# Optimization experiments

Measured on AMD Instinct MI355X. Metric: run time of the kernel, lower is better.

The kernel has to match this reference:

```python
import jax, jax.numpy as jnp
import numpy as np

B, T, C, H = 2, 2048, 1024, 16
D = C // H  # head dim = 64

def setup_inputs() -> dict:
    key = jax.random.key(0)
    ks = jax.random.split(key, 5)
    s = 0.02
    return {
        "x": jax.random.normal(ks[0], (B, T, C), dtype=jnp.float32),
        "Wqkv": jax.random.normal(ks[1], (C, 3 * C), dtype=jnp.float32) * s,
        "bqkv": jnp.zeros((3 * C,), dtype=jnp.float32),
        "Wproj": jax.random.normal(ks[2], (C, C), dtype=jnp.float32) * s,
        "bproj": jnp.zeros((C,), dtype=jnp.float32),
    }

def reference(x, Wqkv, bqkv, Wproj, bproj):
    b, t, c = x.shape
    qkv = x @ Wqkv + bqkv                       # [B,T,3C]
    q, k, v = jnp.split(qkv, 3, axis=-1)
    # [B,T,C] -> [B,H,T,D]
    q = q.reshape(b, t, H, D).transpose(0, 2, 1, 3)
    k = k.reshape(b, t, H, D).transpose(0, 2, 1, 3)
    v = v.reshape(b, t, H, D).transpose(0, 2, 1, 3)
    scale = 1.0 / np.sqrt(D).astype(np.float32)
    attn = jnp.einsum('bhqd,bhkd->bhqk', q, k) * scale  # [B,H,T,T]
    causal = jnp.tril(jnp.ones((t, t), dtype=bool))
    attn = jnp.where(causal, attn, jnp.float32(-jnp.inf))
    attn = jax.nn.softmax(attn, axis=-1)
    y = jnp.einsum('bhqk,bhkd->bhqd', attn, v)          # [B,H,T,D]
    y = y.transpose(0, 2, 1, 3).reshape(b, t, c)        # [B,T,C]
    return y @ Wproj + bproj
```

## Files before the change

### kernel.cpp

```cpp
#include <hip/hip_runtime.h>
#include <stdint.h>

#define B_ 2
#define T_ 2048
#define C_ 1024
#define H_ 16
#define D_ 64
#define M_ (B_*T_)
#define BHTD_ (B_*H_*T_*D_)

typedef __bf16 bf16x8 __attribute__((ext_vector_type(8)));
typedef __bf16 bf16x4 __attribute__((ext_vector_type(4)));
typedef __bf16 bf16x2 __attribute__((ext_vector_type(2)));
typedef float f32x4 __attribute__((ext_vector_type(4)));
typedef float f32x16 __attribute__((ext_vector_type(16)));

static __device__ __forceinline__ unsigned short f32_bf16(float f) {
    unsigned int u = __float_as_uint(f);
    u += 0x7FFFu + ((u >> 16) & 1u);
    return (unsigned short)(u >> 16);
}

static __device__ __forceinline__ int pack_bf16_2(float a, float b) {
    bf16x2 v = {(__bf16)a, (__bf16)b};
    return __builtin_bit_cast(int, v);
}

__global__ void cast_kernel(const float* __restrict__ in, unsigned short* __restrict__ out, int n) {
    int i = (blockIdx.x * 256 + threadIdx.x) * 4;
    if (i >= n) return;
    float4 f = *(const float4*)(in + i);
    ushort4 o;
    o.x = f32_bf16(f.x); o.y = f32_bf16(f.y); o.z = f32_bf16(f.z); o.w = f32_bf16(f.w);
    *(ushort4*)(out + i) = o;
}

__global__ void transpose_cast_kernel(const float* __restrict__ W, unsigned short* __restrict__ Wt,
                                      int K, int N) {
    __shared__ float tile[32][33];
    int n0 = blockIdx.x * 32, k0 = blockIdx.y * 32;
    int tx = threadIdx.x, ty = threadIdx.y;
    #pragma unroll
    for (int j = 0; j < 32; j += 8)
        tile[ty + j][tx] = W[(size_t)(k0 + ty + j) * N + n0 + tx];
    __syncthreads();
    #pragma unroll
    for (int j = 0; j < 32; j += 8)
        Wt[(size_t)(n0 + ty + j) * K + k0 + tx] = f32_bf16(tile[tx][ty + j]);
}

template<int EPI>
__global__ __launch_bounds__(256) void gemm_bt(
    const unsigned short* __restrict__ A,
    const unsigned short* __restrict__ Bt,
    const float* __restrict__ bias,
    unsigned short* __restrict__ out_bf16,
    float* __restrict__ out_f32,
    int M, int N, int K)
{
    __shared__ unsigned short As[2][128 * 32];
    __shared__ unsigned short Bs[2][128 * 32];
    int tid = threadIdx.x;
    int lane = tid & 63, wid = tid >> 6;
    int fr = lane & 15, fg = lane >> 4;
    int row0 = blockIdx.x * 128, col0 = blockIdx.y * 128;
    int wm = (wid >> 1) * 64, wn = (wid & 1) * 64;

    f32x4 acc[4][4];
    #pragma unroll
    for (int i = 0; i < 4; ++i)
        #pragma unroll
        for (int j = 0; j < 4; ++j)
            acc[i][j] = (f32x4){0.f, 0.f, 0.f, 0.f};

    const int srw = lane >> 2;
    const int scl = (lane & 3) * 8;
    const int c0 = wid * 2, c1 = wid * 2 + 1;

    auto stage = [&](int buf, int k0) {
        __builtin_amdgcn_global_load_lds(
            (const __attribute__((address_space(1))) void*)(A + (size_t)(row0 + c0 * 16 + srw) * K + k0 + scl),
            (__attribute__((address_space(3))) void*)(As[buf] + c0 * 512), 16, 0, 0);
        __builtin_amdgcn_global_load_lds(
            (const __attribute__((address_space(1))) void*)(A + (size_t)(row0 + c1 * 16 + srw) * K + k0 + scl),
            (__attribute__((address_space(3))) void*)(As[buf] + c1 * 512), 16, 0, 0);
        __builtin_amdgcn_global_load_lds(
            (const __attribute__((address_space(1))) void*)(Bt + (size_t)(col0 + c0 * 16 + srw) * K + k0 + scl),
            (__attribute__((address_space(3))) void*)(Bs[buf] + c0 * 512), 16, 0, 0);
        __builtin_amdgcn_global_load_lds(
            (const __attribute__((address_space(1))) void*)(Bt + (size_t)(col0 + c1 * 16 + srw) * K + k0 + scl),
            (__attribute__((address_space(3))) void*)(Bs[buf] + c1 * 512), 16, 0, 0);
    };

    stage(0, 0);
    __syncthreads();

    int cur = 0;
    for (int k0 = 0; k0 < K; k0 += 32) {
        if (k0 + 32 < K) stage(cur ^ 1, k0 + 32);

        bf16x8 af[4], bfr[4];
        #pragma unroll
        for (int i = 0; i < 4; ++i) {
            af[i]  = *(const bf16x8*)(As[cur] + (wm + i * 16 + fr) * 32 + fg * 8);
            bfr[i] = *(const bf16x8*)(Bs[cur] + (wn + i * 16 + fr) * 32 + fg * 8);
        }
        #pragma unroll
        for (int mi = 0; mi < 4; ++mi)
            #pragma unroll
            for (int ni = 0; ni < 4; ++ni)
                acc[mi][ni] = __builtin_amdgcn_mfma_f32_16x16x32_bf16(af[mi], bfr[ni], acc[mi][ni], 0, 0, 0);

        __syncthreads();
        cur ^= 1;
    }

    #pragma unroll
    for (int mi = 0; mi < 4; ++mi) {
        int rowb = row0 + wm + mi * 16 + fg * 4;
        #pragma unroll
        for (int ni = 0; ni < 4; ++ni) {
            int col = col0 + wn + ni * 16 + fr;
            float bv = bias[col];
            #pragma unroll
            for (int r = 0; r < 4; ++r) {
                float v = acc[mi][ni][r] + bv;
                int rr = rowb + r;
                if (EPI == 0) {
                    int part = col >> 10, c = col & 1023;
                    int h = c >> 6, d = c & 63;
                    int b = rr >> 11, t = rr & 2047;
                    if (part == 0) v *= 0.18033688011112042f;
                    size_t idx;
                    if (part == 2)
                        idx = (size_t)2 * BHTD_ + ((size_t)(b * H_ + h) * D_ + d) * T_ + t;
                    else
                        idx = (size_t)part * BHTD_ + ((size_t)(b * H_ + h) * T_ + t) * D_ + d;
                    out_bf16[idx] = f32_bf16(v);
                } else {
                    out_f32[(size_t)rr * N + col] = v;
                }
            }
        }
    }
}

__global__ __launch_bounds__(128) void attn_kernel(
    const unsigned short* __restrict__ qg,
    const unsigned short* __restrict__ kg,
    const unsigned short* __restrict__ vtg,
    unsigned short* __restrict__ y)
{
    const int id = blockIdx.x;
    const int xcd = id & 7, j = id >> 3;
    const int c = j & 31, g = j >> 5;
    int chunk;
    if      (g == 0) chunk = 31 - c;
    else if (g == 1) chunk = c;
    else if (g == 2) chunk = (15 - c) & 31;
    else             chunk = (c + 16) & 31;
    const int bh = xcd * 4 + (c >> 3);
    const int b = bh >> 4, h = bh & 15;
    const int tid = threadIdx.x, wid = tid >> 6, lane = tid & 63;
    const int lq = lane & 31, hi = lane >> 5;

    const unsigned short* qp = qg + (size_t)bh * (T_ * D_);
    const char* kpB = (const char*)(kg + (size_t)bh * (T_ * D_));
    const char* vpB = (const char*)(vtg + (size_t)bh * (D_ * T_));

    __shared__ __align__(16) char Ks[2][8192];
    __shared__ __align__(16) char Vs[2][8192];

    const int r0 = chunk * 64 + wid * 32;
    const int ntk = chunk + 1;

    bf16x8 qf[4];
    #pragma unroll
    for (int ds = 0; ds < 4; ++ds)
        qf[ds] = *(const bf16x8*)(qp + (size_t)(r0 + lq) * D_ + ds * 16 + hi * 8);

    f32x16 oT0, oT1;
    #pragma unroll
    for (int e = 0; e < 16; ++e) { oT0[e] = 0.f; oT1[e] = 0.f; }
    float lrun = 0.f;

    const int srow8 = lane >> 3;
    const int scol  = (lane & 7) * 16;
    const int ssw   = srow8 << 4;

    auto stage = [&](int buf, int kv0) {
        #pragma unroll
        for (int blk = 0; blk < 4; ++blk) {
            const int rbase = wid * 32 + blk * 8;
            __builtin_amdgcn_global_load_lds(
                (const __attribute__((address_space(1))) void*)
                    (kpB + (size_t)(kv0 + rbase + srow8) * 128 + (scol ^ ssw)),
                (__attribute__((address_space(3))) void*)(Ks[buf] + rbase * 128), 16, 0, 0);
            __builtin_amdgcn_global_load_lds(
                (const __attribute__((address_space(1))) void*)
                    (vpB + (size_t)(rbase + srow8) * 4096 + kv0 * 2 + (scol ^ ssw)),
                (__attribute__((address_space(3))) void*)(Vs[buf] + rbase * 128), 16, 0, 0);
        }
    };

    auto make_pb = [&](const f32x16& p, int g4a) -> bf16x8 {
        int A0 = pack_bf16_2(p[g4a * 4 + 0], p[g4a * 4 + 1]);
        int A1 = pack_bf16_2(p[g4a * 4 + 2], p[g4a * 4 + 3]);
        int B0 = pack_bf16_2(p[g4a * 4 + 4], p[g4a * 4 + 5]);
        int B1 = pack_bf16_2(p[g4a * 4 + 6], p[g4a * 4 + 7]);
        auto ra = __builtin_amdgcn_permlane32_swap(A0, B0, false, false);
        auto rb = __builtin_amdgcn_permlane32_swap(A1, B1, false, false);
        int4 w;
        w.x = ra[0]; w.y = rb[0]; w.z = ra[1]; w.w = rb[1];
        return __builtin_bit_cast(bf16x8, w);
    };

    stage(0, 0);
    __syncthreads();

    const int lsw = (lq & 7) << 4;
    int cur = 0;
    for (int t = 0; t < ntk; ++t) {
        const int kv0 = t * 64;
        if (t + 1 < ntk) stage(cur ^ 1, kv0 + 64);

        const char* Kb = Ks[cur];
        const char* Vb = Vs[cur];
        const bool diag = (t == chunk);
        const bool do_n1 = !(diag && wid == 0);

        f32x16 s0, s1;
        #pragma unroll
        for (int e = 0; e < 16; ++e) { s0[e] = 0.f; s1[e] = 0.f; }
        #pragma unroll
        for (int ds = 0; ds < 4; ++ds) {
            bf16x8 kf = *(const bf16x8*)(Kb + lq * 128 + ((ds * 32 + hi * 16) ^ lsw));
            s0 = __builtin_amdgcn_mfma_f32_32x32x16_bf16(kf, qf[ds], s0, 0, 0, 0);
        }
        if (do_n1) {
            #pragma unroll
            for (int ds = 0; ds < 4; ++ds) {
                bf16x8 kf = *(const bf16x8*)(Kb + (32 + lq) * 128 + ((ds * 32 + hi * 16) ^ lsw));
                s1 = __builtin_amdgcn_mfma_f32_32x32x16_bf16(kf, qf[ds], s1, 0, 0, 0);
            }
        }

        bf16x8 vf[2][4];
        #pragma unroll
        for (int dd = 0; dd < 2; ++dd)
            #pragma unroll
            for (int st = 0; st < 2; ++st)
                vf[dd][st] = *(const bf16x8*)(Vb + (dd * 32 + lq) * 128 +
                                              ((st * 32 + hi * 16) ^ lsw));
        if (do_n1) {
            #pragma unroll
            for (int dd = 0; dd < 2; ++dd)
                #pragma unroll
                for (int st = 2; st < 4; ++st)
                    vf[dd][st] = *(const bf16x8*)(Vb + (dd * 32 + lq) * 128 +
                                                  ((st * 32 + hi * 16) ^ lsw));
        }

        const int qrow = r0 + lq;
        if (diag && wid == 0) {
            #pragma unroll
            for (int e = 0; e < 16; ++e) {
                const int kvl = (e & 3) + ((e >> 2) << 3) + hi * 4;
                s0[e] = exp2f((kv0 + kvl <= qrow) ? s0[e] : -1e30f);
            }
        } else {
            #pragma unroll
            for (int e = 0; e < 16; ++e) s0[e] = exp2f(s0[e]);
        }
        {
            float a0 = (s0[0] + s0[1]) + (s0[2] + s0[3]);
            float a1 = (s0[4] + s0[5]) + (s0[6] + s0[7]);
            float a2 = (s0[8] + s0[9]) + (s0[10] + s0[11]);
            float a3 = (s0[12] + s0[13]) + (s0[14] + s0[15]);
            lrun += (a0 + a1) + (a2 + a3);
        }
        if (do_n1) {
            if (diag) {
                #pragma unroll
                for (int e = 0; e < 16; ++e) {
                    const int kvl = 32 + (e & 3) + ((e >> 2) << 3) + hi * 4;
                    s1[e] = exp2f((kv0 + kvl <= qrow) ? s1[e] : -1e30f);
                }
            } else {
                #pragma unroll
                for (int e = 0; e < 16; ++e) s1[e] = exp2f(s1[e]);
            }
            float a0 = (s1[0] + s1[1]) + (s1[2] + s1[3]);
            float a1 = (s1[4] + s1[5]) + (s1[6] + s1[7]);
            float a2 = (s1[8] + s1[9]) + (s1[10] + s1[11]);
            float a3 = (s1[12] + s1[13]) + (s1[14] + s1[15]);
            lrun += (a0 + a1) + (a2 + a3);
        }

        {
            bf16x8 pb = make_pb(s0, 0);
            oT0 = __builtin_amdgcn_mfma_f32_32x32x16_bf16(vf[0][0], pb, oT0, 0, 0, 0);
            oT1 = __builtin_amdgcn_mfma_f32_32x32x16_bf16(vf[1][0], pb, oT1, 0, 0, 0);
            pb = make_pb(s0, 2);
            oT0 = __builtin_amdgcn_mfma_f32_32x32x16_bf16(vf[0][1], pb, oT0, 0, 0, 0);
            oT1 = __builtin_amdgcn_mfma_f32_32x32x16_bf16(vf[1][1], pb, oT1, 0, 0, 0);
        }
        if (do_n1) {
            bf16x8 pb = make_pb(s1, 0);
            oT0 = __builtin_amdgcn_mfma_f32_32x32x16_bf16(vf[0][2], pb, oT0, 0, 0, 0);
            oT1 = __builtin_amdgcn_mfma_f32_32x32x16_bf16(vf[1][2], pb, oT1, 0, 0, 0);
            pb = make_pb(s1, 2);
            oT0 = __builtin_amdgcn_mfma_f32_32x32x16_bf16(vf[0][3], pb, oT0, 0, 0, 0);
            oT1 = __builtin_amdgcn_mfma_f32_32x32x16_bf16(vf[1][3], pb, oT1, 0, 0, 0);
        }

        __syncthreads();
        cur ^= 1;
    }

    const float ls = lrun + __shfl_xor(lrun, 32);
    const float inv = 1.f / ls;
    const int trow = r0 + lq;
    unsigned short* yrow = y + ((size_t)b * T_ + trow) * C_ + h * 64;
    #pragma unroll
    for (int dd = 0; dd < 2; ++dd) {
        const f32x16& o = dd ? oT1 : oT0;
        #pragma unroll
        for (int g4 = 0; g4 < 4; ++g4) {
            bf16x4 ov = {(__bf16)(o[g4 * 4 + 0] * inv), (__bf16)(o[g4 * 4 + 1] * inv),
                         (__bf16)(o[g4 * 4 + 2] * inv), (__bf16)(o[g4 * 4 + 3] * inv)};
            *(uint2*)(yrow + dd * 32 + g4 * 8 + hi * 4) = __builtin_bit_cast(uint2, ov);
        }
    }
}

extern "C" void kernel_launch(void* const* d_in, const int* in_sizes, int n_in,
                              void* d_out, int out_size, void* d_ws, size_t ws_size,
                              hipStream_t stream) {
    const float* x     = (const float*)d_in[0];
    const float* Wqkv  = (const float*)d_in[1];
    const float* bqkv  = (const float*)d_in[2];
    const float* Wproj = (const float*)d_in[3];
    const float* bproj = (const float*)d_in[4];
    float* out = (float*)d_out;

    char* ws = (char*)d_ws;
    unsigned short* x_bf    = (unsigned short*)(ws);
    unsigned short* wqkv_t  = (unsigned short*)(ws + 8388608);
    unsigned short* wproj_t = (unsigned short*)(ws + 14680064);
    unsigned short* qkv     = (unsigned short*)(ws + 16777216);
    unsigned short* ybuf    = (unsigned short*)(ws + 41943040);

    cast_kernel<<<(M_ * C_) / 4 / 256, 256, 0, stream>>>(x, x_bf, M_ * C_);
    transpose_cast_kernel<<<dim3(3072 / 32, 1024 / 32), dim3(32, 8), 0, stream>>>(Wqkv, wqkv_t, 1024, 3072);
    transpose_cast_kernel<<<dim3(1024 / 32, 1024 / 32), dim3(32, 8), 0, stream>>>(Wproj, wproj_t, 1024, 1024);

    gemm_bt<0><<<dim3(M_ / 128, 3072 / 128), 256, 0, stream>>>(
        x_bf, wqkv_t, bqkv, qkv, nullptr, M_, 3072, 1024);

    attn_kernel<<<dim3(1024), 128, 0, stream>>>(
        qkv, qkv + (size_t)BHTD_, qkv + 2 * (size_t)BHTD_, ybuf);

    gemm_bt<1><<<dim3(M_ / 128, 1024 / 128), 256, 0, stream>>>(
        ybuf, wproj_t, bproj, nullptr, out, M_, 1024, 1024);
}
```

Before: 134.2 us.

## Pair high and low causal query chunks per block to share KV tiles

Each attention block now holds four waves. Two waves process a high query chunk and two process its mirrored low chunk (p and 31-p), and all four share the same staged K/V tiles in LDS. This balances causal work per block and cuts redundant K/V global loads for the low chunk. The cost is that the low-chunk waves sit idle at the barriers after their chunk finishes, and the grid is halved to 512 blocks of 256 threads.

```diff
diff --git a/kernel.cpp b/kernel.cpp
--- a/kernel.cpp
+++ b/kernel.cpp
@@ -145,21 +145,18 @@
     }
 }
 
-__global__ __launch_bounds__(128) void attn_kernel(
+__global__ __launch_bounds__(256) void attn_kernel(
     const unsigned short* __restrict__ qg,
     const unsigned short* __restrict__ kg,
     const unsigned short* __restrict__ vtg,
     unsigned short* __restrict__ y)
 {
     const int id = blockIdx.x;
-    const int xcd = id & 7, j = id >> 3;
-    const int c = j & 31, g = j >> 5;
-    int chunk;
-    if      (g == 0) chunk = 31 - c;
-    else if (g == 1) chunk = c;
-    else if (g == 2) chunk = (15 - c) & 31;
-    else             chunk = (c + 16) & 31;
-    const int bh = xcd * 4 + (c >> 3);
+    const int xcd = id & 7, loc = id >> 3;
+    const int bh = xcd * 4 + (loc & 3);
+    const int iq = loc >> 2;
+    const int p = (iq < 8) ? iq : 23 - iq;
+    const int chhi = 31 - p, chlo = p;
     const int b = bh >> 4, h = bh & 15;
     const int tid = threadIdx.x, wid = tid >> 6, lane = tid & 63;
     const int lq = lane & 31, hi = lane >> 5;
@@ -171,8 +168,11 @@
     __shared__ __align__(16) char Ks[2][8192];
     __shared__ __align__(16) char Vs[2][8192];
 
-    const int r0 = chunk * 64 + wid * 32;
-    const int ntk = chunk + 1;
+    const int mych = (wid < 2) ? chhi : chlo;
+    const int r0 = mych * 64 + (wid & 1) * 32;
+    const int nthi = chhi + 1;
+    const int ntlo = chlo + 1;
+    const bool is_hi = (wid < 2);
 
     bf16x8 qf[4];
     #pragma unroll
@@ -190,8 +190,8 @@
 
     auto stage = [&](int buf, int kv0) {
         #pragma unroll
-        for (int blk = 0; blk < 4; ++blk) {
-            const int rbase = wid * 32 + blk * 8;
+        for (int bc = 0; bc < 2; ++bc) {
+            const int rbase = wid * 16 + bc * 8;
             __builtin_amdgcn_global_load_lds(
                 (const __attribute__((address_space(1))) void*)
                     (kpB + (size_t)(kv0 + rbase + srow8) * 128 + (scol ^ ssw)),
@@ -203,11 +203,11 @@
         }
     };
 
-    auto make_pb = [&](const f32x16& p, int g4a) -> bf16x8 {
-        int A0 = pack_bf16_2(p[g4a * 4 + 0], p[g4a * 4 + 1]);
-        int A1 = pack_bf16_2(p[g4a * 4 + 2], p[g4a * 4 + 3]);
-        int B0 = pack_bf16_2(p[g4a * 4 + 4], p[g4a * 4 + 5]);
-        int B1 = pack_bf16_2(p[g4a * 4 + 6], p[g4a * 4 + 7]);
+    auto make_pb = [&](const f32x16& p4, int g4a) -> bf16x8 {
+        int A0 = pack_bf16_2(p4[g4a * 4 + 0], p4[g4a * 4 + 1]);
+        int A1 = pack_bf16_2(p4[g4a * 4 + 2], p4[g4a * 4 + 3]);
+        int B0 = pack_bf16_2(p4[g4a * 4 + 4], p4[g4a * 4 + 5]);
+        int B1 = pack_bf16_2(p4[g4a * 4 + 6], p4[g4a * 4 + 7]);
         auto ra = __builtin_amdgcn_permlane32_swap(A0, B0, false, false);
         auto rb = __builtin_amdgcn_permlane32_swap(A1, B1, false, false);
         int4 w;
@@ -220,98 +220,107 @@
 
     const int lsw = (lq & 7) << 4;
     int cur = 0;
-    for (int t = 0; t < ntk; ++t) {
+    for (int t = 0; t < nthi; ++t) {
         const int kv0 = t * 64;
-        if (t + 1 < ntk) stage(cur ^ 1, kv0 + 64);
-
-        const char* Kb = Ks[cur];
-        const char* Vb = Vs[cur];
-        const bool diag = (t == chunk);
-        const bool do_n1 = !(diag && wid == 0);
-
-        f32x16 s0, s1;
-        #pragma unroll
-        for (int e = 0; e < 16; ++e) { s0[e] = 0.f; s1[e] = 0.f; }
-        #pragma unroll
-        for (int ds = 0; ds < 4; ++ds) {
-            bf16x8 kf = *(const bf16x8*)(Kb + lq * 128 + ((ds * 32 + hi * 16) ^ lsw));
-            s0 = __builtin_amdgcn_mfma_f32_32x32x16_bf16(kf, qf[ds], s0, 0, 0, 0);
-        }
-        if (do_n1) {
+        if (t + 1 < nthi) stage(cur ^ 1, kv0 + 64);
+
+        const bool active = is_hi || (t < ntlo);
+        if (active) {
+            const char* Kb = Ks[cur];
+            const char* Vb = Vs[cur];
+            const bool diag = (t == mych);
+            const bool do_n1 = !(diag && (wid & 1) == 0);
+
+            f32x16 s0, s1;
+            #pragma unroll
+            for (int e = 0; e < 16; ++e) { s0[e] = 0.f; s1[e] = 0.f; }
             #pragma unroll
             for (int ds = 0; ds < 4; ++ds) {
-                bf16x8 kf = *(const bf16x8*)(Kb + (32 + lq) * 128 + ((ds * 32 + hi * 16) ^ lsw));
-                s1 = __builtin_amdgcn_mfma_f32_32x32x16_bf16(kf, qf[ds], s1, 0, 0, 0);
-            }
-        }
-
-        bf16x8 vf[2][4];
-        #pragma unroll
-        for (int dd = 0; dd < 2; ++dd)
-            #pragma unroll
-            for (int st = 0; st < 2; ++st)
-                vf[dd][st] = *(const bf16x8*)(Vb + (dd * 32 + lq) * 128 +
-                                              ((st * 32 + hi * 16) ^ lsw));
-        if (do_n1) {
+                bf16x8 kf = *(const bf16x8*)(Kb + lq * 128 + ((ds * 32 + hi * 16) ^ lsw));
+                s0 = __builtin_amdgcn_mfma_f32_32x32x16_bf16(kf, qf[ds], s0, 0, 0, 0);
+            }
+            if (do_n1) {
+                #pragma unroll
+                for (int ds = 0; ds < 4; ++ds) {
+                    bf16x8 kf = *(const bf16x8*)(Kb + (32 + lq) * 128 + ((ds * 32 + hi * 16) ^ lsw));
+                    s1 = __builtin_amdgcn_mfma_f32_32x32x16_bf16(kf, qf[ds], s1, 0, 0, 0);
+                }
+            }
+
+            bf16x8 vf[2][4];
             #pragma unroll
             for (int dd = 0; dd < 2; ++dd)
                 #pragma unroll
-                for (int st = 2; st < 4; ++st)
+                for (int st = 0; st < 2; ++st)
                     vf[dd][st] = *(const bf16x8*)(Vb + (dd * 32 + lq) * 128 +
                                                   ((st * 32 + hi * 16) ^ lsw));
-        }
-
-        const int qrow = r0 + lq;
-        if (diag && wid == 0) {
-            #pragma unroll
-            for (int e = 0; e < 16; ++e) {
-                const int kvl = (e & 3) + ((e >> 2) << 3) + hi * 4;
-                s0[e] = exp2f((kv0 + kvl <= qrow) ? s0[e] : -1e30f);
-            }
-        } else {
-            #pragma unroll
-            for (int e = 0; e < 16; ++e) s0[e] = exp2f(s0[e]);
-        }
-        {
-            float a0 = (s0[0] + s0[1]) + (s0[2] + s0[3]);
-            float a1 = (s0[4] + s0[5]) + (s0[6] + s0[7]);
-            float a2 = (s0[8] + s0[9]) + (s0[10] + s0[11]);
-            float a3 = (s0[12] + s0[13]) + (s0[14] + s0[15]);
-            lrun += (a0 + a1) + (a2 + a3);
-        }
-        if (do_n1) {
-            if (diag) {
+            if (do_n1) {
+                #pragma unroll
+                for (int dd = 0; dd < 2; ++dd)
+                    #pragma unroll
+                    for (int st = 2; st < 4; ++st)
+                        vf[dd][st] = *(const bf16x8*)(Vb + (dd * 32 + lq) * 128 +
+                                                      ((st * 32 + hi * 16) ^ lsw));
+            }
+
+            const int qrow = r0 + lq;
+            if (diag && (wid & 1) == 0) {
                 #pragma unroll
                 for (int e = 0; e < 16; ++e) {
-                    const int kvl = 32 + (e & 3) + ((e >> 2) << 3) + hi * 4;
-                    s1[e] = exp2f((kv0 + kvl <= qrow) ? s1[e] : -1e30f);
+                    const int kvl = (e & 3) + ((e >> 2) << 3) + hi * 4;
+                    s0[e] = exp2f((kv0 + kvl <= qrow) ? s0[e] : -1e30f);
+                }
+            } else if (diag) {
+                #pragma unroll
+                for (int e = 0; e < 16; ++e) {
+                    const int kvl = (e & 3) + ((e >> 2) << 3) + hi * 4;
+                    s0[e] = exp2f((kv0 + kvl <= qrow) ? s0[e] : -1e30f);
                 }
             } else {
                 #pragma unroll
-                for (int e = 0; e < 16; ++e) s1[e] = exp2f(s1[e]);
-            }
-            float a0 = (s1[0] + s1[1]) + (s1[2] + s1[3]);
-            float a1 = (s1[4] + s1[5]) + (s1[6] + s1[7]);
-            float a2 = (s1[8] + s1[9]) + (s1[10] + s1[11]);
-            float a3 = (s1[12] + s1[13]) + (s1[14] + s1[15]);
-            lrun += (a0 + a1) + (a2 + a3);
-        }
-
-        {
-            bf16x8 pb = make_pb(s0, 0);
-            oT0 = __builtin_amdgcn_mfma_f32_32x32x16_bf16(vf[0][0], pb, oT0, 0, 0, 0);
-            oT1 = __builtin_amdgcn_mfma_f32_32x32x16_bf16(vf[1][0], pb, oT1, 0, 0, 0);
-            pb = make_pb(s0, 2);
-            oT0 = __builtin_amdgcn_mfma_f32_32x32x16_bf16(vf[0][1], pb, oT0, 0, 0, 0);
-            oT1 = __builtin_amdgcn_mfma_f32_32x32x16_bf16(vf[1][1], pb, oT1, 0, 0, 0);
-        }
-        if (do_n1) {
-            bf16x8 pb = make_pb(s1, 0);
-            oT0 = __builtin_amdgcn_mfma_f32_32x32x16_bf16(vf[0][2], pb, oT0, 0, 0, 0);
-            oT1 = __builtin_amdgcn_mfma_f32_32x32x16_bf16(vf[1][2], pb, oT1, 0, 0, 0);
-            pb = make_pb(s1, 2);
-            oT0 = __builtin_amdgcn_mfma_f32_32x32x16_bf16(vf[0][3], pb, oT0, 0, 0, 0);
-            oT1 = __builtin_amdgcn_mfma_f32_32x32x16_bf16(vf[1][3], pb, oT1, 0, 0, 0);
+                for (int e = 0; e < 16; ++e) s0[e] = exp2f(s0[e]);
+            }
+            {
+                float a0 = (s0[0] + s0[1]) + (s0[2] + s0[3]);
+                float a1 = (s0[4] + s0[5]) + (s0[6] + s0[7]);
+                float a2 = (s0[8] + s0[9]) + (s0[10] + s0[11]);
+                float a3 = (s0[12] + s0[13]) + (s0[14] + s0[15]);
+                lrun += (a0 + a1) + (a2 + a3);
+            }
+            if (do_n1) {
+                if (diag) {
+                    #pragma unroll
+                    for (int e = 0; e < 16; ++e) {
+                        const int kvl = 32 + (e & 3) + ((e >> 2) << 3) + hi * 4;
+                        s1[e] = exp2f((kv0 + kvl <= qrow) ? s1[e] : -1e30f);
+                    }
+                } else {
+                    #pragma unroll
+                    for (int e = 0; e < 16; ++e) s1[e] = exp2f(s1[e]);
+                }
+                float a0 = (s1[0] + s1[1]) + (s1[2] + s1[3]);
+                float a1 = (s1[4] + s1[5]) + (s1[6] + s1[7]);
+                float a2 = (s1[8] + s1[9]) + (s1[10] + s1[11]);
+                float a3 = (s1[12] + s1[13]) + (s1[14] + s1[15]);
+                lrun += (a0 + a1) + (a2 + a3);
+            }
+
+            {
+                bf16x8 pb = make_pb(s0, 0);
+                oT0 = __builtin_amdgcn_mfma_f32_32x32x16_bf16(vf[0][0], pb, oT0, 0, 0, 0);
+                oT1 = __builtin_amdgcn_mfma_f32_32x32x16_bf16(vf[1][0], pb, oT1, 0, 0, 0);
+                pb = make_pb(s0, 2);
+                oT0 = __builtin_amdgcn_mfma_f32_32x32x16_bf16(vf[0][1], pb, oT0, 0, 0, 0);
+                oT1 = __builtin_amdgcn_mfma_f32_32x32x16_bf16(vf[1][1], pb, oT1, 0, 0, 0);
+            }
+            if (do_n1) {
+                bf16x8 pb = make_pb(s1, 0);
+                oT0 = __builtin_amdgcn_mfma_f32_32x32x16_bf16(vf[0][2], pb, oT0, 0, 0, 0);
+                oT1 = __builtin_amdgcn_mfma_f32_32x32x16_bf16(vf[1][2], pb, oT1, 0, 0, 0);
+                pb = make_pb(s1, 2);
+                oT0 = __builtin_amdgcn_mfma_f32_32x32x16_bf16(vf[0][3], pb, oT0, 0, 0, 0);
+                oT1 = __builtin_amdgcn_mfma_f32_32x32x16_bf16(vf[1][3], pb, oT1, 0, 0, 0);
+            }
         }
 
         __syncthreads();
@@ -358,7 +367,7 @@
     gemm_bt<0><<<dim3(M_ / 128, 3072 / 128), 256, 0, stream>>>(
         x_bf, wqkv_t, bqkv, qkv, nullptr, M_, 3072, 1024);
 
-    attn_kernel<<<dim3(1024), 128, 0, stream>>>(
+    attn_kernel<<<dim3(512), 256, 0, stream>>>(
         qkv, qkv + (size_t)BHTD_, qkv + 2 * (size_t)BHTD_, ybuf);
 
     gemm_bt<1><<<dim3(M_ / 128, 1024 / 128), 256, 0, stream>>>(
```

Measured after the change: 135.0 us. No clear change (+0.6%).
